# Performance work log

Hardware: AMD Instinct MI355X
Metric: run time of the kernel (lower is better)

## Reference

```python
import jax, jax.numpy as jnp
import numpy as np

B, LQ, LK, D = 8, 2048, 2048, 64
TEMPERATURE = 8.0  # sqrt(D)


def setup_inputs() -> dict:
    key = jax.random.key(0)
    ks = jax.random.split(key, 9)
    q = jax.random.normal(ks[0], (B, LQ, D), dtype=jnp.float32)
    k = jax.random.normal(ks[1], (B, LK, D), dtype=jnp.float32)
    v = jax.random.normal(ks[2], (B, LK, D), dtype=jnp.float32)
    mask = jax.random.randint(ks[3], (B, LQ, LK), 0, 2).astype(jnp.bool_)
    f1 = jax.random.normal(ks[4], (B, LQ, LK), dtype=jnp.float32)
    f2 = jax.random.normal(ks[5], (B, LQ, LK), dtype=jnp.float32)
    f3 = jax.random.normal(ks[6], (B, LQ, LK), dtype=jnp.float32)
    f4 = jax.random.normal(ks[7], (B, LQ, LK), dtype=jnp.float32)
    f5 = jax.random.normal(ks[8], (B, LQ, LK), dtype=jnp.float32)
    return {"q": q, "k": k, "v": v, "mask": mask,
            "tf_f1_features": f1, "tf_f2_features": f2, "tf_f3_features": f3,
            "tf_f4_features": f4, "tf_f5_features": f5}


def reference(q, k, v, mask, tf_f1_features, tf_f2_features, tf_f3_features,
              tf_f4_features, tf_f5_features):
    # scores: [B, Lq, Lk]
    attn = jnp.einsum("bqd,bkd->bqk", q, k)
    attn = attn + tf_f1_features + tf_f2_features + tf_f3_features + tf_f4_features + tf_f5_features
    attn = attn / TEMPERATURE
    attn = jnp.where(mask, -jnp.inf, attn)
    attn = jax.nn.softmax(attn, axis=2)
    # dropout is identity (attn_dropout=0 / eval mode)
    output = jnp.einsum("bqk,bkd->bqd", attn, v)
    return (output, attn)
```

## Files before the change

kernel.cpp:

```cpp
#include <hip/hip_runtime.h>


#define BBn 8
#define LQn 2048
#define LKn 2048
#define DDn 64

typedef _Float16 half8 __attribute__((ext_vector_type(8)));
typedef _Float16 half4 __attribute__((ext_vector_type(4)));
typedef float floatx4 __attribute__((ext_vector_type(4)));
typedef int intx4 __attribute__((ext_vector_type(4)));

__global__ __launch_bounds__(256) void detect_mask(const unsigned* __restrict__ m,
                                                   int* __restrict__ flag) {
  __shared__ int s_int, s_f32;
  const int tid = threadIdx.x;
  if (tid == 0) { s_int = 1; s_f32 = 1; }
  __syncthreads();
  int oki = 1, okf = 1;
  for (int i = tid; i < 4096; i += 256) {
    unsigned x = m[i];
    oki &= (x <= 1u);
    okf &= (x == 0u || x == 0x3f800000u);
  }
  atomicAnd(&s_int, oki);
  atomicAnd(&s_f32, okf);
  __syncthreads();
  if (tid == 0) *flag = s_int ? 0 : (s_f32 ? 1 : 2);
}

__global__ __launch_bounds__(512, 4) void attn_logits(
    const float* __restrict__ qp, const float* __restrict__ kp,
    const float* __restrict__ f1, const float* __restrict__ f2,
    const float* __restrict__ f3, const float* __restrict__ f4,
    const float* __restrict__ f5,
    const void* __restrict__ maskp, const int* __restrict__ flag,
    float* __restrict__ attn, float* __restrict__ invl) {
  const int blk = blockIdx.x;
  const int b   = blk >> 7;
  const int q0  = (blk & 127) << 4;
  const int tid = threadIdx.x;
  const int w   = tid >> 6;
  const int l   = tid & 63;
  const int lr  = l & 15;
  const int lgp = l >> 4;
  const int mode = *flag;

  const float* qrow = qp + ((size_t)(b * LQn + q0 + lr)) * DDn;
  half8 aq[2];
#pragma unroll
  for (int dc = 0; dc < 2; ++dc) {
    floatx4 x0 = *(const floatx4*)(qrow + dc * 32 + lgp * 8);
    floatx4 x1 = *(const floatx4*)(qrow + dc * 32 + lgp * 8 + 4);
    half8 h;
#pragma unroll
    for (int i = 0; i < 4; ++i) { h[i] = (_Float16)x0[i]; h[i + 4] = (_Float16)x1[i]; }
    aq[dc] = h;
  }

  float lsum[4] = {0.f, 0.f, 0.f, 0.f};
  const size_t rowbase = (size_t)b * LQn + q0;
  const int t0 = w * 256;

  for (int kb = t0; kb < t0 + 256; kb += 64) {
    floatx4 acc[4];
#pragma unroll
    for (int jj = 0; jj < 4; ++jj) acc[jj] = (floatx4){0.f, 0.f, 0.f, 0.f};
#pragma unroll
    for (int dc = 0; dc < 2; ++dc) {
#pragma unroll
      for (int jj = 0; jj < 4; ++jj) {
        const float* krow =
            kp + ((size_t)(b * LKn + kb + 4 * lr + jj)) * DDn + dc * 32 + lgp * 8;
        floatx4 x0 = *(const floatx4*)(krow);
        floatx4 x1 = *(const floatx4*)(krow + 4);
        half8 h;
#pragma unroll
        for (int i = 0; i < 4; ++i) { h[i] = (_Float16)x0[i]; h[i + 4] = (_Float16)x1[i]; }
        acc[jj] = __builtin_amdgcn_mfma_f32_16x16x32_f16(aq[dc], h, acc[jj], 0, 0, 0);
      }
    }
#pragma unroll
    for (int r = 0; r < 4; ++r) {
      const int row = lgp * 4 + r;
      const size_t fof = (rowbase + row) * (size_t)LKn + (size_t)(kb + 4 * lr);
      floatx4 v1 = *(const floatx4*)(f1 + fof);
      floatx4 v2 = *(const floatx4*)(f2 + fof);
      floatx4 v3 = *(const floatx4*)(f3 + fof);
      floatx4 v4 = *(const floatx4*)(f4 + fof);
      floatx4 v5 = *(const floatx4*)(f5 + fof);
      int msk[4];
      if (mode == 0) {
        intx4 m4 = *(const intx4*)((const int*)maskp + fof);
        msk[0] = (m4[0] != 0); msk[1] = (m4[1] != 0);
        msk[2] = (m4[2] != 0); msk[3] = (m4[3] != 0);
      } else if (mode == 1) {
        floatx4 m4 = *(const floatx4*)((const float*)maskp + fof);
        msk[0] = (m4[0] != 0.f); msk[1] = (m4[1] != 0.f);
        msk[2] = (m4[2] != 0.f); msk[3] = (m4[3] != 0.f);
      } else {
        unsigned mv = *(const unsigned*)((const unsigned char*)maskp + fof);
        msk[0] = (int)(mv & 0xffu); msk[1] = (int)((mv >> 8) & 0xffu);
        msk[2] = (int)((mv >> 16) & 0xffu); msk[3] = (int)((mv >> 24) & 0xffu);
      }
      floatx4 ev;
#pragma unroll
      for (int jj = 0; jj < 4; ++jj) {
        float lgt = (acc[jj][r] + v1[jj] + v2[jj] + v3[jj] + v4[jj] + v5[jj]) * 0.125f;
        float e = msk[jj] ? 0.f : __expf(lgt - 16.f);
        ev[jj] = e;
        lsum[r] += e;
      }
      *(floatx4*)(attn + fof) = ev;
    }
  }

#pragma unroll
  for (int off = 1; off < 16; off <<= 1) {
#pragma unroll
    for (int r = 0; r < 4; ++r) lsum[r] += __shfl_xor(lsum[r], off);
  }
  __shared__ float lds_l[8][16];
  if (lr == 0) {
#pragma unroll
    for (int r = 0; r < 4; ++r) lds_l[w][lgp * 4 + r] = lsum[r];
  }
  __syncthreads();
  if (tid < 16) {
    float s = 0.f;
#pragma unroll
    for (int ww = 0; ww < 8; ++ww) s += lds_l[ww][tid];
    invl[rowbase + tid] = 1.0f / s;
  }
}

__global__ __launch_bounds__(256, 4) void attn_pv(
    const float* __restrict__ vp, const float* __restrict__ invl,
    float* __restrict__ attn, float* __restrict__ outp) {
  const int blk = blockIdx.x;
  const int b   = blk >> 7;
  const int q0  = (blk & 127) << 4;
  const int tid = threadIdx.x;
  const int w   = tid >> 6;
  const int l   = tid & 63;
  const int lr  = l & 15;
  const int lgp = l >> 4;

  __shared__ __align__(16) _Float16 p16[4][16][72];
  __shared__ float osum[4][16][64];

  const size_t rowbase = (size_t)b * LQn + q0;
  float il[4];
#pragma unroll
  for (int r = 0; r < 4; ++r) il[r] = invl[rowbase + lgp * 4 + r];

  floatx4 acc[4];
#pragma unroll
  for (int dt = 0; dt < 4; ++dt) acc[dt] = (floatx4){0.f, 0.f, 0.f, 0.f};

  const int t0 = w * 512;
  for (int kb = t0; kb < t0 + 512; kb += 64) {
#pragma unroll
    for (int r = 0; r < 4; ++r) {
      const int row = lgp * 4 + r;
      const size_t fof = (rowbase + row) * (size_t)LKn + (size_t)(kb + 4 * lr);
      floatx4 e = *(const floatx4*)(attn + fof);
      floatx4 p = e * il[r];
      *(floatx4*)(attn + fof) = p;
      half4 hp;
#pragma unroll
      for (int jj = 0; jj < 4; ++jj) hp[jj] = (_Float16)p[jj];
      *(half4*)(&p16[w][row][4 * lr]) = hp;
    }
    half8 pa[2];
#pragma unroll
    for (int tc = 0; tc < 2; ++tc)
      pa[tc] = *(const half8*)(&p16[w][lr][tc * 32 + lgp * 8]);
#pragma unroll
    for (int tc = 0; tc < 2; ++tc) {
#pragma unroll
      for (int dt = 0; dt < 4; ++dt) {
        const float* vbase =
            vp + ((size_t)(b * LKn + kb + tc * 32 + lgp * 8)) * DDn + dt * 16 + lr;
        half8 bv;
#pragma unroll
        for (int i = 0; i < 8; ++i) bv[i] = (_Float16)vbase[i * DDn];
        acc[dt] = __builtin_amdgcn_mfma_f32_16x16x32_f16(pa[tc], bv, acc[dt], 0, 0, 0);
      }
    }
  }

#pragma unroll
  for (int dt = 0; dt < 4; ++dt) {
#pragma unroll
    for (int r = 0; r < 4; ++r) osum[w][lgp * 4 + r][dt * 16 + lr] = acc[dt][r];
  }
  __syncthreads();
#pragma unroll
  for (int ii = 0; ii < 4; ++ii) {
    int idx = tid + 256 * ii;
    int row = idx >> 6, d = idx & 63;
    float s = osum[0][row][d] + osum[1][row][d] + osum[2][row][d] + osum[3][row][d];
    outp[(rowbase + row) * DDn + d] = s;
  }
}

extern "C" void kernel_launch(void* const* d_in, const int* in_sizes, int n_in,
                              void* d_out, int out_size, void* d_ws, size_t ws_size,
                              hipStream_t stream) {
  const float* q  = (const float*)d_in[0];
  const float* k  = (const float*)d_in[1];
  const float* v  = (const float*)d_in[2];
  const void*  mask = d_in[3];
  const float* f1 = (const float*)d_in[4];
  const float* f2 = (const float*)d_in[5];
  const float* f3 = (const float*)d_in[6];
  const float* f4 = (const float*)d_in[7];
  const float* f5 = (const float*)d_in[8];

  float* outp = (float*)d_out;
  float* attn = outp + (size_t)BBn * LQn * DDn;
  float* invl = (float*)d_ws;
  int*   flag = (int*)d_ws + (BBn * LQn);

  detect_mask<<<1, 256, 0, stream>>>((const unsigned*)mask, flag);
  attn_logits<<<1024, 512, 0, stream>>>(q, k, f1, f2, f3, f4, f5, mask, flag, attn, invl);
  attn_pv<<<1024, 256, 0, stream>>>(v, invl, attn, outp);
}
```

Baseline: 296.7 us.

## Pre-convert K/V to fp16 with MFMA-friendly V layout and widen logits tile

Adds a prep kernel that converts K to fp16 and repacks V into the exact per-lane fragment layout the PV MFMA consumes, and folds mask-type detection into the same launch. The logits kernel now handles 32 query rows per block and reuses each K fragment for two MFMAs, halving K reloads. The PV kernel loads contiguous half8 V fragments instead of eight strided fp32 loads. The original kernels are kept as a fallback for a small workspace, at the cost of an extra prep pass and more workspace.

New measurement: 294.5 us. No clear change (-0.7%).

```diff
diff --git a/kernel.cpp b/kernel.cpp
--- a/kernel.cpp
+++ b/kernel.cpp
@@ -10,6 +10,53 @@
 typedef _Float16 half4 __attribute__((ext_vector_type(4)));
 typedef float floatx4 __attribute__((ext_vector_type(4)));
 typedef int intx4 __attribute__((ext_vector_type(4)));
+
+__global__ __launch_bounds__(256) void prep_all(
+    const float* __restrict__ kp, const float* __restrict__ vp,
+    const unsigned* __restrict__ m, _Float16* __restrict__ kh,
+    _Float16* __restrict__ vh, int* __restrict__ flag) {
+  const int blk = blockIdx.x;
+  const int tid = threadIdx.x;
+  if (blk < 512) {
+    const size_t off = ((size_t)blk * 256 + tid) * 8;
+    floatx4 x0 = *(const floatx4*)(kp + off);
+    floatx4 x1 = *(const floatx4*)(kp + off + 4);
+    half8 h;
+#pragma unroll
+    for (int i = 0; i < 4; ++i) { h[i] = (_Float16)x0[i]; h[i + 4] = (_Float16)x1[i]; }
+    *(half8*)(kh + off) = h;
+  } else if (blk < 1024) {
+    int fid = (blk - 512) * 256 + tid;
+    const int lr  = fid & 15;  fid >>= 4;
+    const int lgp = fid & 3;   fid >>= 2;
+    const int dt  = fid & 3;   fid >>= 2;
+    const int tc  = fid & 1;   fid >>= 1;
+    const int kb6 = fid & 31;  fid >>= 5;
+    const int b   = fid;
+    const float* vbase =
+        vp + ((size_t)(b * LKn + kb6 * 64 + tc * 32 + lgp * 8)) * DDn + dt * 16 + lr;
+    half8 h;
+#pragma unroll
+    for (int i = 0; i < 8; ++i) h[i] = (_Float16)vbase[i * DDn];
+    const size_t vof =
+        ((((((size_t)b * 32 + kb6) * 2 + tc) * 4 + dt) * 4 + lgp) * 16 + lr) * 8;
+    *(half8*)(vh + vof) = h;
+  } else {
+    __shared__ int s_int, s_f32;
+    if (tid == 0) { s_int = 1; s_f32 = 1; }
+    __syncthreads();
+    int oki = 1, okf = 1;
+    for (int i = tid; i < 4096; i += 256) {
+      unsigned x = m[i];
+      oki &= (x <= 1u);
+      okf &= (x == 0u || x == 0x3f800000u);
+    }
+    atomicAnd(&s_int, oki);
+    atomicAnd(&s_f32, okf);
+    __syncthreads();
+    if (tid == 0) *flag = s_int ? 0 : (s_f32 ? 1 : 2);
+  }
+}
 
 __global__ __launch_bounds__(256) void detect_mask(const unsigned* __restrict__ m,
                                                    int* __restrict__ flag) {
@@ -29,7 +76,190 @@
   if (tid == 0) *flag = s_int ? 0 : (s_f32 ? 1 : 2);
 }
 
-__global__ __launch_bounds__(512, 4) void attn_logits(
+__global__ __launch_bounds__(512, 4) void attn_logits32(
+    const float* __restrict__ qp, const _Float16* __restrict__ kh,
+    const float* __restrict__ f1, const float* __restrict__ f2,
+    const float* __restrict__ f3, const float* __restrict__ f4,
+    const float* __restrict__ f5,
+    const void* __restrict__ maskp, const int* __restrict__ flag,
+    float* __restrict__ attn, float* __restrict__ invl) {
+  const int blk = blockIdx.x;
+  const int b   = blk >> 6;
+  const int q0  = (blk & 63) << 5;
+  const int tid = threadIdx.x;
+  const int w   = tid >> 6;
+  const int l   = tid & 63;
+  const int lr  = l & 15;
+  const int lgp = l >> 4;
+  const int mode = *flag;
+
+  half8 aq[2][2];
+#pragma unroll
+  for (int t = 0; t < 2; ++t) {
+    const float* qrow = qp + ((size_t)(b * LQn + q0 + t * 16 + lr)) * DDn;
+#pragma unroll
+    for (int dc = 0; dc < 2; ++dc) {
+      floatx4 x0 = *(const floatx4*)(qrow + dc * 32 + lgp * 8);
+      floatx4 x1 = *(const floatx4*)(qrow + dc * 32 + lgp * 8 + 4);
+      half8 h;
+#pragma unroll
+      for (int i = 0; i < 4; ++i) { h[i] = (_Float16)x0[i]; h[i + 4] = (_Float16)x1[i]; }
+      aq[t][dc] = h;
+    }
+  }
+
+  float lsum[2][4] = {{0.f, 0.f, 0.f, 0.f}, {0.f, 0.f, 0.f, 0.f}};
+  const size_t rowbase = (size_t)b * LQn + q0;
+  const int t0 = w * 256;
+
+  for (int kb = t0; kb < t0 + 256; kb += 64) {
+    floatx4 acc[2][4];
+#pragma unroll
+    for (int t = 0; t < 2; ++t)
+#pragma unroll
+      for (int jj = 0; jj < 4; ++jj) acc[t][jj] = (floatx4){0.f, 0.f, 0.f, 0.f};
+#pragma unroll
+    for (int dc = 0; dc < 2; ++dc) {
+#pragma unroll
+      for (int jj = 0; jj < 4; ++jj) {
+        half8 bk = *(const half8*)(
+            kh + ((size_t)(b * LKn + kb + 4 * lr + jj)) * DDn + dc * 32 + lgp * 8);
+#pragma unroll
+        for (int t = 0; t < 2; ++t)
+          acc[t][jj] = __builtin_amdgcn_mfma_f32_16x16x32_f16(aq[t][dc], bk, acc[t][jj], 0, 0, 0);
+      }
+    }
+#pragma unroll
+    for (int t = 0; t < 2; ++t) {
+#pragma unroll
+      for (int r = 0; r < 4; ++r) {
+        const int row = t * 16 + lgp * 4 + r;
+        const size_t fof = (rowbase + row) * (size_t)LKn + (size_t)(kb + 4 * lr);
+        floatx4 v1 = *(const floatx4*)(f1 + fof);
+        floatx4 v2 = *(const floatx4*)(f2 + fof);
+        floatx4 v3 = *(const floatx4*)(f3 + fof);
+        floatx4 v4 = *(const floatx4*)(f4 + fof);
+        floatx4 v5 = *(const floatx4*)(f5 + fof);
+        int msk[4];
+        if (mode == 0) {
+          intx4 m4 = *(const intx4*)((const int*)maskp + fof);
+          msk[0] = (m4[0] != 0); msk[1] = (m4[1] != 0);
+          msk[2] = (m4[2] != 0); msk[3] = (m4[3] != 0);
+        } else if (mode == 1) {
+          floatx4 m4 = *(const floatx4*)((const float*)maskp + fof);
+          msk[0] = (m4[0] != 0.f); msk[1] = (m4[1] != 0.f);
+          msk[2] = (m4[2] != 0.f); msk[3] = (m4[3] != 0.f);
+        } else {
+          unsigned mv = *(const unsigned*)((const unsigned char*)maskp + fof);
+          msk[0] = (int)(mv & 0xffu); msk[1] = (int)((mv >> 8) & 0xffu);
+          msk[2] = (int)((mv >> 16) & 0xffu); msk[3] = (int)((mv >> 24) & 0xffu);
+        }
+        floatx4 ev;
+#pragma unroll
+        for (int jj = 0; jj < 4; ++jj) {
+          float lgt = (acc[t][jj][r] + v1[jj] + v2[jj] + v3[jj] + v4[jj] + v5[jj]) * 0.125f;
+          float e = msk[jj] ? 0.f : __expf(lgt - 16.f);
+          ev[jj] = e;
+          lsum[t][r] += e;
+        }
+        *(floatx4*)(attn + fof) = ev;
+      }
+    }
+  }
+
+#pragma unroll
+  for (int off = 1; off < 16; off <<= 1) {
+#pragma unroll
+    for (int t = 0; t < 2; ++t)
+#pragma unroll
+      for (int r = 0; r < 4; ++r) lsum[t][r] += __shfl_xor(lsum[t][r], off);
+  }
+  __shared__ float lds_l[8][32];
+  if (lr == 0) {
+#pragma unroll
+    for (int t = 0; t < 2; ++t)
+#pragma unroll
+      for (int r = 0; r < 4; ++r) lds_l[w][t * 16 + lgp * 4 + r] = lsum[t][r];
+  }
+  __syncthreads();
+  if (tid < 32) {
+    float s = 0.f;
+#pragma unroll
+    for (int ww = 0; ww < 8; ++ww) s += lds_l[ww][tid];
+    invl[rowbase + tid] = 1.0f / s;
+  }
+}
+
+__global__ __launch_bounds__(256, 4) void attn_pv(
+    const _Float16* __restrict__ vh, const float* __restrict__ invl,
+    float* __restrict__ attn, float* __restrict__ outp) {
+  const int blk = blockIdx.x;
+  const int b   = blk >> 7;
+  const int q0  = (blk & 127) << 4;
+  const int tid = threadIdx.x;
+  const int w   = tid >> 6;
+  const int l   = tid & 63;
+  const int lr  = l & 15;
+  const int lgp = l >> 4;
+
+  __shared__ __align__(16) _Float16 p16[4][16][72];
+  __shared__ float osum[4][16][64];
+
+  const size_t rowbase = (size_t)b * LQn + q0;
+  float il[4];
+#pragma unroll
+  for (int r = 0; r < 4; ++r) il[r] = invl[rowbase + lgp * 4 + r];
+
+  floatx4 acc[4];
+#pragma unroll
+  for (int dt = 0; dt < 4; ++dt) acc[dt] = (floatx4){0.f, 0.f, 0.f, 0.f};
+
+  const int t0 = w * 512;
+  for (int kb = t0; kb < t0 + 512; kb += 64) {
+    const int kb6 = kb >> 6;
+#pragma unroll
+    for (int r = 0; r < 4; ++r) {
+      const int row = lgp * 4 + r;
+      const size_t fof = (rowbase + row) * (size_t)LKn + (size_t)(kb + 4 * lr);
+      floatx4 e = *(const floatx4*)(attn + fof);
+      floatx4 p = e * il[r];
+      *(floatx4*)(attn + fof) = p;
+      half4 hp;
+#pragma unroll
+      for (int jj = 0; jj < 4; ++jj) hp[jj] = (_Float16)p[jj];
+      *(half4*)(&p16[w][row][4 * lr]) = hp;
+    }
+    half8 pa[2];
+#pragma unroll
+    for (int tc = 0; tc < 2; ++tc)
+      pa[tc] = *(const half8*)(&p16[w][lr][tc * 32 + lgp * 8]);
+#pragma unroll
+    for (int tc = 0; tc < 2; ++tc) {
+#pragma unroll
+      for (int dt = 0; dt < 4; ++dt) {
+        half8 bv = *(const half8*)(
+            vh + ((((((size_t)b * 32 + kb6) * 2 + tc) * 4 + dt) * 4 + lgp) * 16 + lr) * 8);
+        acc[dt] = __builtin_amdgcn_mfma_f32_16x16x32_f16(pa[tc], bv, acc[dt], 0, 0, 0);
+      }
+    }
+  }
+
+#pragma unroll
+  for (int dt = 0; dt < 4; ++dt) {
+#pragma unroll
+    for (int r = 0; r < 4; ++r) osum[w][lgp * 4 + r][dt * 16 + lr] = acc[dt][r];
+  }
+  __syncthreads();
+#pragma unroll
+  for (int ii = 0; ii < 4; ++ii) {
+    int idx = tid + 256 * ii;
+    int row = idx >> 6, d = idx & 63;
+    float s = osum[0][row][d] + osum[1][row][d] + osum[2][row][d] + osum[3][row][d];
+    outp[(rowbase + row) * DDn + d] = s;
+  }
+}
+
+__global__ __launch_bounds__(512, 4) void attn_logits_fb(
     const float* __restrict__ qp, const float* __restrict__ kp,
     const float* __restrict__ f1, const float* __restrict__ f2,
     const float* __restrict__ f3, const float* __restrict__ f4,
@@ -45,7 +275,6 @@
   const int lr  = l & 15;
   const int lgp = l >> 4;
   const int mode = *flag;
-
   const float* qrow = qp + ((size_t)(b * LQn + q0 + lr)) * DDn;
   half8 aq[2];
 #pragma unroll
@@ -57,11 +286,9 @@
     for (int i = 0; i < 4; ++i) { h[i] = (_Float16)x0[i]; h[i + 4] = (_Float16)x1[i]; }
     aq[dc] = h;
   }
-
   float lsum[4] = {0.f, 0.f, 0.f, 0.f};
   const size_t rowbase = (size_t)b * LQn + q0;
   const int t0 = w * 256;
-
   for (int kb = t0; kb < t0 + 256; kb += 64) {
     floatx4 acc[4];
 #pragma unroll
@@ -114,7 +341,6 @@
       *(floatx4*)(attn + fof) = ev;
     }
   }
-
 #pragma unroll
   for (int off = 1; off < 16; off <<= 1) {
 #pragma unroll
@@ -134,7 +360,7 @@
   }
 }
 
-__global__ __launch_bounds__(256, 4) void attn_pv(
+__global__ __launch_bounds__(256, 4) void attn_pv_fb(
     const float* __restrict__ vp, const float* __restrict__ invl,
     float* __restrict__ attn, float* __restrict__ outp) {
   const int blk = blockIdx.x;
@@ -145,19 +371,15 @@
   const int l   = tid & 63;
   const int lr  = l & 15;
   const int lgp = l >> 4;
-
   __shared__ __align__(16) _Float16 p16[4][16][72];
   __shared__ float osum[4][16][64];
-
   const size_t rowbase = (size_t)b * LQn + q0;
   float il[4];
 #pragma unroll
   for (int r = 0; r < 4; ++r) il[r] = invl[rowbase + lgp * 4 + r];
-
   floatx4 acc[4];
 #pragma unroll
   for (int dt = 0; dt < 4; ++dt) acc[dt] = (floatx4){0.f, 0.f, 0.f, 0.f};
-
   const int t0 = w * 512;
   for (int kb = t0; kb < t0 + 512; kb += 64) {
 #pragma unroll
@@ -189,7 +411,6 @@
       }
     }
   }
-
 #pragma unroll
   for (int dt = 0; dt < 4; ++dt) {
 #pragma unroll
@@ -220,10 +441,21 @@
 
   float* outp = (float*)d_out;
   float* attn = outp + (size_t)BBn * LQn * DDn;
+
+  const size_t KH_OFF = 131072, VH_OFF = KH_OFF + 2097152, NEED = VH_OFF + 2097152;
   float* invl = (float*)d_ws;
-  int*   flag = (int*)d_ws + (BBn * LQn);
-
-  detect_mask<<<1, 256, 0, stream>>>((const unsigned*)mask, flag);
-  attn_logits<<<1024, 512, 0, stream>>>(q, k, f1, f2, f3, f4, f5, mask, flag, attn, invl);
-  attn_pv<<<1024, 256, 0, stream>>>(v, invl, attn, outp);
-}
+  int*   flag = (int*)((char*)d_ws + 65536);
+  _Float16* kh = (_Float16*)((char*)d_ws + KH_OFF);
+  _Float16* vh = (_Float16*)((char*)d_ws + VH_OFF);
+
+  if (ws_size >= NEED) {
+    prep_all<<<1025, 256, 0, stream>>>(k, v, (const unsigned*)mask, kh, vh, flag);
+    attn_logits32<<<512, 512, 0, stream>>>(q, kh, f1, f2, f3, f4, f5, mask, flag, attn, invl);
+    attn_pv<<<1024, 256, 0, stream>>>(vh, invl, attn, outp);
+  } else {
+    int* flag2 = (int*)d_ws + (BBn * LQn);
+    detect_mask<<<1, 256, 0, stream>>>((const unsigned*)mask, flag2);
+    attn_logits_fb<<<1024, 512, 0, stream>>>(q, k, f1, f2, f3, f4, f5, mask, flag2, attn, invl);
+    attn_pv_fb<<<1024, 256, 0, stream>>>(v, invl, attn, outp);
+  }
+}
```

## Split logits into scores/exp kernels with fp16 scratch and pre-packed V

Applied to the files above, without the earlier changes.

Restructures the pipeline into four kernels. A prep kernel converts V to fp16 in MFMA-ready layout, a scores kernel computes QK^T for 32-row tiles into an fp16 workspace buffer, a row-wise kernel adds the five feature tensors, applies the mask and exponentiates, and the PV kernel reads the fp16 probabilities and packed V. The goal is to cut the strided V loads and the fp32 attention intermediate traffic, and to give the bandwidth-bound exp pass better occupancy. In exchange it adds an extra full-size fp16 round trip and launch, and fp16 storage of exp values, with a fixed shift of 5, risks overflow or precision loss.

Result: slower. 314.6 us (+6.0%).

```diff
diff --git a/kernel.cpp b/kernel.cpp
--- a/kernel.cpp
+++ b/kernel.cpp
@@ -11,31 +11,193 @@
 typedef float floatx4 __attribute__((ext_vector_type(4)));
 typedef int intx4 __attribute__((ext_vector_type(4)));
 
-__global__ __launch_bounds__(256) void detect_mask(const unsigned* __restrict__ m,
-                                                   int* __restrict__ flag) {
-  __shared__ int s_int, s_f32;
+__global__ __launch_bounds__(256) void prep_v(
+    const float* __restrict__ vp, const unsigned* __restrict__ m,
+    _Float16* __restrict__ vh, int* __restrict__ flag) {
+  const int blk = blockIdx.x;
   const int tid = threadIdx.x;
-  if (tid == 0) { s_int = 1; s_f32 = 1; }
-  __syncthreads();
-  int oki = 1, okf = 1;
-  for (int i = tid; i < 4096; i += 256) {
-    unsigned x = m[i];
-    oki &= (x <= 1u);
-    okf &= (x == 0u || x == 0x3f800000u);
-  }
-  atomicAnd(&s_int, oki);
-  atomicAnd(&s_f32, okf);
-  __syncthreads();
-  if (tid == 0) *flag = s_int ? 0 : (s_f32 ? 1 : 2);
-}
-
-__global__ __launch_bounds__(512, 4) void attn_logits(
+  if (blk < 512) {
+    int fid = blk * 256 + tid;
+    const int lr  = fid & 15;  fid >>= 4;
+    const int lgp = fid & 3;   fid >>= 2;
+    const int dt  = fid & 3;   fid >>= 2;
+    const int tc  = fid & 1;   fid >>= 1;
+    const int kb6 = fid & 31;  fid >>= 5;
+    const int b   = fid;
+    const float* vbase =
+        vp + ((size_t)(b * LKn + kb6 * 64 + tc * 32 + lgp * 8)) * DDn + dt * 16 + lr;
+    half8 h;
+#pragma unroll
+    for (int i = 0; i < 8; ++i) h[i] = (_Float16)vbase[i * DDn];
+    const size_t vof =
+        ((((((size_t)b * 32 + kb6) * 2 + tc) * 4 + dt) * 4 + lgp) * 16 + lr) * 8;
+    *(half8*)(vh + vof) = h;
+  } else {
+    __shared__ int s_int, s_f32;
+    if (tid == 0) { s_int = 1; s_f32 = 1; }
+    __syncthreads();
+    int oki = 1, okf = 1;
+    for (int i = tid; i < 4096; i += 256) {
+      unsigned x = m[i];
+      oki &= (x <= 1u);
+      okf &= (x == 0u || x == 0x3f800000u);
+    }
+    atomicAnd(&s_int, oki);
+    atomicAnd(&s_f32, okf);
+    __syncthreads();
+    if (tid == 0) *flag = s_int ? 0 : (s_f32 ? 1 : 2);
+  }
+}
+
+__global__ __launch_bounds__(512, 2) void attn_scores(
     const float* __restrict__ qp, const float* __restrict__ kp,
+    _Float16* __restrict__ s16, float* __restrict__ s32, const int use16) {
+  const int blk = blockIdx.x;
+  const int b   = blk >> 6;
+  const int q0  = (blk & 63) << 5;
+  const int tid = threadIdx.x;
+  const int w   = tid >> 6;
+  const int l   = tid & 63;
+  const int lr  = l & 15;
+  const int lgp = l >> 4;
+
+  half8 aq[2][2];
+#pragma unroll
+  for (int t = 0; t < 2; ++t) {
+    const float* qrow = qp + ((size_t)(b * LQn + q0 + t * 16 + lr)) * DDn;
+#pragma unroll
+    for (int dc = 0; dc < 2; ++dc) {
+      floatx4 x0 = *(const floatx4*)(qrow + dc * 32 + lgp * 8);
+      floatx4 x1 = *(const floatx4*)(qrow + dc * 32 + lgp * 8 + 4);
+      half8 h;
+#pragma unroll
+      for (int i = 0; i < 4; ++i) { h[i] = (_Float16)x0[i]; h[i + 4] = (_Float16)x1[i]; }
+      aq[t][dc] = h;
+    }
+  }
+
+  const size_t rowbase = (size_t)b * LQn + q0;
+  const int t0 = w * 256;
+
+  for (int kb = t0; kb < t0 + 256; kb += 64) {
+    floatx4 acc[2][4];
+#pragma unroll
+    for (int t = 0; t < 2; ++t)
+#pragma unroll
+      for (int jj = 0; jj < 4; ++jj) acc[t][jj] = (floatx4){0.f, 0.f, 0.f, 0.f};
+#pragma unroll
+    for (int dc = 0; dc < 2; ++dc) {
+#pragma unroll
+      for (int jj = 0; jj < 4; ++jj) {
+        const float* krow =
+            kp + ((size_t)(b * LKn + kb + 4 * lr + jj)) * DDn + dc * 32 + lgp * 8;
+        floatx4 x0 = *(const floatx4*)(krow);
+        floatx4 x1 = *(const floatx4*)(krow + 4);
+        half8 h;
+#pragma unroll
+        for (int i = 0; i < 4; ++i) { h[i] = (_Float16)x0[i]; h[i + 4] = (_Float16)x1[i]; }
+#pragma unroll
+        for (int t = 0; t < 2; ++t)
+          acc[t][jj] = __builtin_amdgcn_mfma_f32_16x16x32_f16(aq[t][dc], h, acc[t][jj], 0, 0, 0);
+      }
+    }
+#pragma unroll
+    for (int t = 0; t < 2; ++t) {
+#pragma unroll
+      for (int r = 0; r < 4; ++r) {
+        const size_t off = (rowbase + t * 16 + lgp * 4 + r) * (size_t)LKn
+                         + (size_t)(kb + 4 * lr);
+        if (use16) {
+          half4 hp;
+#pragma unroll
+          for (int jj = 0; jj < 4; ++jj) hp[jj] = (_Float16)acc[t][jj][r];
+          *(half4*)(s16 + off) = hp;
+        } else {
+          floatx4 ev;
+#pragma unroll
+          for (int jj = 0; jj < 4; ++jj) ev[jj] = acc[t][jj][r];
+          *(floatx4*)(s32 + off) = ev;
+        }
+      }
+    }
+  }
+}
+
+__global__ __launch_bounds__(256, 8) void attn_exp(
     const float* __restrict__ f1, const float* __restrict__ f2,
     const float* __restrict__ f3, const float* __restrict__ f4,
     const float* __restrict__ f5,
     const void* __restrict__ maskp, const int* __restrict__ flag,
-    float* __restrict__ attn, float* __restrict__ invl) {
+    _Float16* __restrict__ s16, float* __restrict__ s32, const int use16,
+    float* __restrict__ invl) {
+  const int row = blockIdx.x;
+  const size_t base = (size_t)row * (size_t)LKn;
+  const int tid = threadIdx.x;
+  const int mode = *flag;
+  float sum = 0.f;
+
+#pragma unroll
+  for (int kk = 0; kk < 2; ++kk) {
+    const size_t off = base + (size_t)(kk * 1024 + 4 * tid);
+    float sv[4];
+    if (use16) {
+      half4 h = *(const half4*)(s16 + off);
+#pragma unroll
+      for (int j = 0; j < 4; ++j) sv[j] = (float)h[j];
+    } else {
+      floatx4 x = *(const floatx4*)(s32 + off);
+#pragma unroll
+      for (int j = 0; j < 4; ++j) sv[j] = x[j];
+    }
+    floatx4 v1 = *(const floatx4*)(f1 + off);
+    floatx4 v2 = *(const floatx4*)(f2 + off);
+    floatx4 v3 = *(const floatx4*)(f3 + off);
+    floatx4 v4 = *(const floatx4*)(f4 + off);
+    floatx4 v5 = *(const floatx4*)(f5 + off);
+    int msk[4];
+    if (mode == 0) {
+      intx4 m4 = *(const intx4*)((const int*)maskp + off);
+      msk[0] = (m4[0] != 0); msk[1] = (m4[1] != 0);
+      msk[2] = (m4[2] != 0); msk[3] = (m4[3] != 0);
+    } else if (mode == 1) {
+      floatx4 m4 = *(const floatx4*)((const float*)maskp + off);
+      msk[0] = (m4[0] != 0.f); msk[1] = (m4[1] != 0.f);
+      msk[2] = (m4[2] != 0.f); msk[3] = (m4[3] != 0.f);
+    } else {
+      unsigned mv = *(const unsigned*)((const unsigned char*)maskp + off);
+      msk[0] = (int)(mv & 0xffu); msk[1] = (int)((mv >> 8) & 0xffu);
+      msk[2] = (int)((mv >> 16) & 0xffu); msk[3] = (int)((mv >> 24) & 0xffu);
+    }
+    floatx4 ev;
+#pragma unroll
+    for (int j = 0; j < 4; ++j) {
+      float lgt = (sv[j] + v1[j] + v2[j] + v3[j] + v4[j] + v5[j]) * 0.125f;
+      float e = msk[j] ? 0.f : __expf(lgt - 5.f);
+      ev[j] = e;
+      sum += e;
+    }
+    if (use16) {
+      half4 hp;
+#pragma unroll
+      for (int j = 0; j < 4; ++j) hp[j] = (_Float16)ev[j];
+      *(half4*)(s16 + off) = hp;
+    } else {
+      *(floatx4*)(s32 + off) = ev;
+    }
+  }
+
+#pragma unroll
+  for (int o = 1; o < 64; o <<= 1) sum += __shfl_xor(sum, o);
+  __shared__ float ls[4];
+  if ((tid & 63) == 0) ls[tid >> 6] = sum;
+  __syncthreads();
+  if (tid == 0) invl[row] = 1.0f / (ls[0] + ls[1] + ls[2] + ls[3]);
+}
+
+__global__ __launch_bounds__(256, 4) void attn_pv(
+    const _Float16* __restrict__ vh, const float* __restrict__ invl,
+    const _Float16* __restrict__ s16, float* __restrict__ attn, const int use16,
+    float* __restrict__ outp) {
   const int blk = blockIdx.x;
   const int b   = blk >> 7;
   const int q0  = (blk & 127) << 4;
@@ -44,128 +206,35 @@
   const int l   = tid & 63;
   const int lr  = l & 15;
   const int lgp = l >> 4;
-  const int mode = *flag;
-
-  const float* qrow = qp + ((size_t)(b * LQn + q0 + lr)) * DDn;
-  half8 aq[2];
-#pragma unroll
-  for (int dc = 0; dc < 2; ++dc) {
-    floatx4 x0 = *(const floatx4*)(qrow + dc * 32 + lgp * 8);
-    floatx4 x1 = *(const floatx4*)(qrow + dc * 32 + lgp * 8 + 4);
-    half8 h;
-#pragma unroll
-    for (int i = 0; i < 4; ++i) { h[i] = (_Float16)x0[i]; h[i + 4] = (_Float16)x1[i]; }
-    aq[dc] = h;
-  }
-
-  float lsum[4] = {0.f, 0.f, 0.f, 0.f};
+
+  __shared__ __align__(16) _Float16 p16[4][16][72];
+  __shared__ float osum[4][16][64];
+
   const size_t rowbase = (size_t)b * LQn + q0;
-  const int t0 = w * 256;
-
-  for (int kb = t0; kb < t0 + 256; kb += 64) {
-    floatx4 acc[4];
-#pragma unroll
-    for (int jj = 0; jj < 4; ++jj) acc[jj] = (floatx4){0.f, 0.f, 0.f, 0.f};
-#pragma unroll
-    for (int dc = 0; dc < 2; ++dc) {
-#pragma unroll
-      for (int jj = 0; jj < 4; ++jj) {
-        const float* krow =
-            kp + ((size_t)(b * LKn + kb + 4 * lr + jj)) * DDn + dc * 32 + lgp * 8;
-        floatx4 x0 = *(const floatx4*)(krow);
-        floatx4 x1 = *(const floatx4*)(krow + 4);
-        half8 h;
-#pragma unroll
-        for (int i = 0; i < 4; ++i) { h[i] = (_Float16)x0[i]; h[i + 4] = (_Float16)x1[i]; }
-        acc[jj] = __builtin_amdgcn_mfma_f32_16x16x32_f16(aq[dc], h, acc[jj], 0, 0, 0);
-      }
-    }
+  float il[4];
+#pragma unroll
+  for (int r = 0; r < 4; ++r) il[r] = invl[rowbase + lgp * 4 + r];
+
+  floatx4 acc[4];
+#pragma unroll
+  for (int dt = 0; dt < 4; ++dt) acc[dt] = (floatx4){0.f, 0.f, 0.f, 0.f};
+
+  const int t0 = w * 512;
+  for (int kb = t0; kb < t0 + 512; kb += 64) {
+    const int kb6 = kb >> 6;
 #pragma unroll
     for (int r = 0; r < 4; ++r) {
       const int row = lgp * 4 + r;
       const size_t fof = (rowbase + row) * (size_t)LKn + (size_t)(kb + 4 * lr);
-      floatx4 v1 = *(const floatx4*)(f1 + fof);
-      floatx4 v2 = *(const floatx4*)(f2 + fof);
-      floatx4 v3 = *(const floatx4*)(f3 + fof);
-      floatx4 v4 = *(const floatx4*)(f4 + fof);
-      floatx4 v5 = *(const floatx4*)(f5 + fof);
-      int msk[4];
-      if (mode == 0) {
-        intx4 m4 = *(const intx4*)((const int*)maskp + fof);
-        msk[0] = (m4[0] != 0); msk[1] = (m4[1] != 0);
-        msk[2] = (m4[2] != 0); msk[3] = (m4[3] != 0);
-      } else if (mode == 1) {
-        floatx4 m4 = *(const floatx4*)((const float*)maskp + fof);
-        msk[0] = (m4[0] != 0.f); msk[1] = (m4[1] != 0.f);
-        msk[2] = (m4[2] != 0.f); msk[3] = (m4[3] != 0.f);
+      floatx4 p;
+      if (use16) {
+        half4 h = *(const half4*)(s16 + fof);
+#pragma unroll
+        for (int jj = 0; jj < 4; ++jj) p[jj] = (float)h[jj] * il[r];
       } else {
-        unsigned mv = *(const unsigned*)((const unsigned char*)maskp + fof);
-        msk[0] = (int)(mv & 0xffu); msk[1] = (int)((mv >> 8) & 0xffu);
-        msk[2] = (int)((mv >> 16) & 0xffu); msk[3] = (int)((mv >> 24) & 0xffu);
+        floatx4 e = *(const floatx4*)(attn + fof);
+        p = e * il[r];
       }
-      floatx4 ev;
-#pragma unroll
-      for (int jj = 0; jj < 4; ++jj) {
-        float lgt = (acc[jj][r] + v1[jj] + v2[jj] + v3[jj] + v4[jj] + v5[jj]) * 0.125f;
-        float e = msk[jj] ? 0.f : __expf(lgt - 16.f);
-        ev[jj] = e;
-        lsum[r] += e;
-      }
-      *(floatx4*)(attn + fof) = ev;
-    }
-  }
-
-#pragma unroll
-  for (int off = 1; off < 16; off <<= 1) {
-#pragma unroll
-    for (int r = 0; r < 4; ++r) lsum[r] += __shfl_xor(lsum[r], off);
-  }
-  __shared__ float lds_l[8][16];
-  if (lr == 0) {
-#pragma unroll
-    for (int r = 0; r < 4; ++r) lds_l[w][lgp * 4 + r] = lsum[r];
-  }
-  __syncthreads();
-  if (tid < 16) {
-    float s = 0.f;
-#pragma unroll
-    for (int ww = 0; ww < 8; ++ww) s += lds_l[ww][tid];
-    invl[rowbase + tid] = 1.0f / s;
-  }
-}
-
-__global__ __launch_bounds__(256, 4) void attn_pv(
-    const float* __restrict__ vp, const float* __restrict__ invl,
-    float* __restrict__ attn, float* __restrict__ outp) {
-  const int blk = blockIdx.x;
-  const int b   = blk >> 7;
-  const int q0  = (blk & 127) << 4;
-  const int tid = threadIdx.x;
-  const int w   = tid >> 6;
-  const int l   = tid & 63;
-  const int lr  = l & 15;
-  const int lgp = l >> 4;
-
-  __shared__ __align__(16) _Float16 p16[4][16][72];
-  __shared__ float osum[4][16][64];
-
-  const size_t rowbase = (size_t)b * LQn + q0;
-  float il[4];
-#pragma unroll
-  for (int r = 0; r < 4; ++r) il[r] = invl[rowbase + lgp * 4 + r];
-
-  floatx4 acc[4];
-#pragma unroll
-  for (int dt = 0; dt < 4; ++dt) acc[dt] = (floatx4){0.f, 0.f, 0.f, 0.f};
-
-  const int t0 = w * 512;
-  for (int kb = t0; kb < t0 + 512; kb += 64) {
-#pragma unroll
-    for (int r = 0; r < 4; ++r) {
-      const int row = lgp * 4 + r;
-      const size_t fof = (rowbase + row) * (size_t)LKn + (size_t)(kb + 4 * lr);
-      floatx4 e = *(const floatx4*)(attn + fof);
-      floatx4 p = e * il[r];
       *(floatx4*)(attn + fof) = p;
       half4 hp;
 #pragma unroll
@@ -180,11 +249,8 @@
     for (int tc = 0; tc < 2; ++tc) {
 #pragma unroll
       for (int dt = 0; dt < 4; ++dt) {
-        const float* vbase =
-            vp + ((size_t)(b * LKn + kb + tc * 32 + lgp * 8)) * DDn + dt * 16 + lr;
-        half8 bv;
-#pragma unroll
-        for (int i = 0; i < 8; ++i) bv[i] = (_Float16)vbase[i * DDn];
+        half8 bv = *(const half8*)(
+            vh + ((((((size_t)b * 32 + kb6) * 2 + tc) * 4 + dt) * 4 + lgp) * 16 + lr) * 8);
         acc[dt] = __builtin_amdgcn_mfma_f32_16x16x32_f16(pa[tc], bv, acc[dt], 0, 0, 0);
       }
     }
@@ -220,10 +286,20 @@
 
   float* outp = (float*)d_out;
   float* attn = outp + (size_t)BBn * LQn * DDn;
+
+  const size_t VH_OFF = 131072;
+  const size_t S16_OFF = VH_OFF + 2097152;
+  const size_t S16_BYTES = (size_t)BBn * LQn * LKn * 2;
+  const size_t NEED16 = S16_OFF + S16_BYTES;
   float* invl = (float*)d_ws;
-  int*   flag = (int*)d_ws + (BBn * LQn);
-
-  detect_mask<<<1, 256, 0, stream>>>((const unsigned*)mask, flag);
-  attn_logits<<<1024, 512, 0, stream>>>(q, k, f1, f2, f3, f4, f5, mask, flag, attn, invl);
-  attn_pv<<<1024, 256, 0, stream>>>(v, invl, attn, outp);
-}
+  int*   flag = (int*)((char*)d_ws + 65536);
+  _Float16* vh  = (_Float16*)((char*)d_ws + VH_OFF);
+  _Float16* s16 = (_Float16*)((char*)d_ws + S16_OFF);
+  const int use16 = (ws_size >= NEED16) ? 1 : 0;
+
+  prep_v<<<513, 256, 0, stream>>>(v, (const unsigned*)mask, vh, flag);
+  attn_scores<<<512, 512, 0, stream>>>(q, k, s16, attn, use16);
+  attn_exp<<<16384, 256, 0, stream>>>(f1, f2, f3, f4, f5, mask, flag,
+                                      s16, attn, use16, invl);
+  attn_pv<<<1024, 256, 0, stream>>>(vh, invl, s16, attn, use16, outp);
+}
```
